# Kernel optimization log

Hardware: AMD Instinct MI355X
Metric: run time of the kernel (lower is better)

Reference implementation:

```python
import jax, jax.numpy as jnp
import numpy as np

S, B, H, T = 1024, 32, 1024, 512


def setup_inputs() -> dict:
    key = jax.random.key(0)
    ks = jax.random.split(key, 7)
    scale = 1.0 / np.sqrt(H)
    return {
        "hidden": jax.random.normal(ks[0], (S, B, H), dtype=jnp.float32),
        "x": jax.random.normal(ks[1], (B, T, H), dtype=jnp.float32),
        "problem_q": jax.random.normal(ks[2], (B, H), dtype=jnp.float32),
        "K_w": jax.random.normal(ks[3], (H, H), dtype=jnp.float32) * scale,
        "K_b": jax.random.normal(ks[4], (H,), dtype=jnp.float32) * scale,
        "V_w": jax.random.normal(ks[5], (H, H), dtype=jnp.float32) * scale,
        "V_b": jax.random.normal(ks[6], (H,), dtype=jnp.float32) * scale,
    }


def reference(hidden, x, problem_q, K_w, K_b, V_w, V_b):
    # hidden: [S, B, H] -> hidden2: [B, S, H]
    hidden2 = jnp.transpose(hidden, (1, 0, 2))
    # Linear projections (torch Linear: y = x @ W.T + b)
    k = jnp.einsum("bsh,kh->bsk", hidden2, K_w) + K_b  # [B, S, H]
    v = jnp.einsum("bsh,kh->bsk", hidden2, V_w) + V_b  # [B, S, H]
    # scores[b,t,s] = x[b,t] . k[b,s]  (QK^T per batch)
    scores = jnp.einsum("bth,bsh->bts", x, k)
    attn = jax.nn.softmax(scores, axis=-1)  # softmax over encoder positions S
    out = jax.nn.sigmoid(jnp.einsum("bts,bsh->bth", attn, v))  # [B, T, H]
    return out
```

## Files before the change

### kernel.cpp

```cpp
#include <hip/hip_runtime.h>

typedef unsigned short u16;
typedef __attribute__((ext_vector_type(8))) short short8;
typedef __attribute__((ext_vector_type(8))) _Float16 half8;
typedef __attribute__((ext_vector_type(4))) float f32x4;
typedef __attribute__((ext_vector_type(4))) u16 u16x4;
typedef __attribute__((ext_vector_type(4))) unsigned int u32x4;

#define DEVINL static __device__ __forceinline__

DEVINL u16 f2bf(float f) {
  unsigned u = __builtin_bit_cast(unsigned, f);
  u += 0x7fffu + ((u >> 16) & 1u);
  return (u16)(u >> 16);
}
DEVINL float bf2f(u16 h) {
  return __builtin_bit_cast(float, ((unsigned)h) << 16);
}
DEVINL u16 f2h(float f) { return __builtin_bit_cast(u16, (_Float16)f); }
DEVINL float h2f(u16 h) { return (float)__builtin_bit_cast(_Float16, h); }

DEVINL void gload16(const void* g, void* l) {
  __builtin_amdgcn_global_load_lds(
      (const __attribute__((address_space(1))) void*)g,
      (__attribute__((address_space(3))) void*)l, 16, 0, 0);
}

#define BAR() asm volatile("s_barrier" ::: "memory")
#define WAIT_VMN(n) asm volatile("s_waitcnt vmcnt(" #n ")" ::: "memory")


__global__ __launch_bounds__(256) void cvt_hidden2_k(const float* __restrict__ hid,
                                                     u16* __restrict__ hf,
                                                     u16* __restrict__ hT) {
  __shared__ u16 tl[64][72];
  const int s0 = blockIdx.x * 64;
  const int h0 = blockIdx.y * 64;
  const int b = blockIdx.z;
  const int t = threadIdx.x;
  const int r = t >> 4;
  const int c4 = (t & 15) * 4;
#pragma unroll
  for (int it = 0; it < 4; ++it) {
    const int s = it * 16 + r;
    const f32x4 v = *(const f32x4*)(hid + ((size_t)(s0 + s) * 32 + b) * 1024 + h0 + c4);
    u16x4 of;
    const int cs = c4 ^ (it << 2);
#pragma unroll
    for (int j = 0; j < 4; ++j) {
      of[j] = f2h(v[j]);
      tl[s][cs + j] = f2bf(v[j]);
    }
    *(u16x4*)(hf + ((size_t)b * 1024 + s0 + s) * 1024 + h0 + c4) = of;
  }
  __syncthreads();
  const int h = t >> 2;
  const int sq = (t & 3) * 16;
  u16 tmp[16] __attribute__((aligned(16)));
#pragma unroll
  for (int i = 0; i < 16; ++i)
    tmp[i] = tl[sq + i][h ^ ((((sq + i) >> 4) & 3) << 2)];
  u16* dst = hT + ((size_t)b * 1024 + h0 + h) * 1024 + s0 + sq;
  *(u32x4*)(dst) = *(const u32x4*)&tmp[0];
  *(u32x4*)(dst + 8) = *(const u32x4*)&tmp[8];
}

__global__ __launch_bounds__(256) void cvt_split_h_k(const float* __restrict__ in,
                                                     u16* __restrict__ hi_o,
                                                     u16* __restrict__ lo_o, long n4) {
  long i = (long)blockIdx.x * 256 + threadIdx.x;
  const long stride = (long)gridDim.x * 256;
  for (; i < n4; i += stride) {
    const f32x4 v = ((const f32x4*)in)[i];
    u16x4 oh, ol;
#pragma unroll
    for (int j = 0; j < 4; ++j) {
      const u16 hi = f2h(v[j]);
      oh[j] = hi;
      ol[j] = f2h(v[j] - h2f(hi));
    }
    ((u16x4*)hi_o)[i] = oh;
    ((u16x4*)lo_o)[i] = ol;
  }
}

__global__ __launch_bounds__(256) void cvt_f32_bf16_k(const float* __restrict__ in,
                                                      u16* __restrict__ out, long n4) {
  long i = (long)blockIdx.x * 256 + threadIdx.x;
  const long stride = (long)gridDim.x * 256;
  for (; i < n4; i += stride) {
    const f32x4 v = ((const f32x4*)in)[i];
    u16x4 o;
#pragma unroll
    for (int j = 0; j < 4; ++j) o[j] = f2bf(v[j]);
    ((u16x4*)out)[i] = o;
  }
}

__global__ __launch_bounds__(256) void cvt_w_t_h_k(const float* __restrict__ in,
                                                   u16* __restrict__ out) {
  __shared__ float tile[64][65];
  const int bh = blockIdx.x * 64;
  const int bj = blockIdx.y * 64;
  const int t = threadIdx.x;
  const int r = t >> 4;
  const int c4 = (t & 15) * 4;
#pragma unroll
  for (int it = 0; it < 4; ++it) {
    const int row = it * 16 + r;
    const f32x4 v = *(const f32x4*)(in + (size_t)(bj + row) * 1024 + bh + c4);
#pragma unroll
    for (int j = 0; j < 4; ++j) tile[c4 + j][row] = v[j];
  }
  __syncthreads();
#pragma unroll
  for (int it = 0; it < 4; ++it) {
    const int hrow = it * 16 + r;
    u16x4 of;
#pragma unroll
    for (int j = 0; j < 4; ++j) of[j] = f2h(tile[hrow][c4 + j]);
    *(u16x4*)(out + (size_t)(bh + hrow) * 1024 + bj + c4) = of;
  }
}

template <int CM>
__global__ __launch_bounds__(512) void gemm2_8ph_k(
    const u16* __restrict__ Ah_, const u16* __restrict__ Al_,
    const u16* __restrict__ B_, void* __restrict__ C0, void* __restrict__ C1) {
  __shared__ u16 lA[3][256 * 64];
  __shared__ u16 lB[3][256 * 32];
  const int bid = blockIdx.x;
  const int swz = (bid & 7) * 32 + (bid >> 3);
  int m0, n0;
  const u16 *Ah, *Al, *Bm;
  float* Cf = nullptr;
  u16 *Chi = nullptr, *Clo = nullptr;
  if (CM == 0) {
    m0 = (swz >> 2) * 256;
    n0 = (swz & 3) * 256;
    Ah = Ah_; Al = Al_; Bm = B_;
    Chi = (u16*)C0; Clo = (u16*)C1;
  } else {
    const int z = swz >> 3;
    m0 = ((swz >> 2) & 1) * 256;
    n0 = (swz & 3) * 256;
    Ah = Ah_ + (size_t)z * 512 * 1024;
    Al = Al_ + (size_t)z * 512 * 1024;
    Bm = B_ + (size_t)z * 1024 * 1024;
    Cf = (float*)C0 + (size_t)z * 512 * 1024;
  }
  const int tid = threadIdx.x;
  const int lane = tid & 63, wid = tid >> 6;
  const int wr = wid >> 2, wc = wid & 3;
  const int fr = lane & 15, fk = lane >> 4;

  f32x4 acc[8][4] = {};

#define STAGEA(pb, kt)                                                         \
  {                                                                            \
    _Pragma("unroll") for (int j = 0; j < 4; ++j) {                            \
      const int slot = j * 512 + tid;                                          \
      const int r = slot >> 3;                                                 \
      const int g = (slot & 7) ^ (r & 7);                                      \
      const u16* src = (g < 4) ? Ah : Al;                                      \
      gload16(src + (size_t)(m0 + r) * 1024 + (kt) * 32 + (g & 3) * 8,         \
              &lA[pb][(j * 512 + wid * 64) * 8]);                              \
    }                                                                          \
  }
#define STAGEB(pb, kt)                                                         \
  {                                                                            \
    _Pragma("unroll") for (int j = 0; j < 2; ++j) {                            \
      const int slot = j * 512 + tid;                                          \
      const int r = slot >> 2;                                                 \
      const int g = (slot & 3) ^ ((r >> 1) & 3);                               \
      gload16(Bm + (size_t)(n0 + r) * 1024 + (kt) * 32 + g * 8,                \
              &lB[pb][(j * 512 + wid * 64) * 8]);                              \
    }                                                                          \
  }

  STAGEA(0, 0);
  STAGEB(0, 0);
  STAGEA(1, 1);
  STAGEB(1, 1);

  int cur = 0;
  for (int t = 0; t < 32; ++t) {
    if (t < 31) {
      WAIT_VMN(6);
    } else {
      WAIT_VMN(0);
    }
    BAR();
    int pre = cur + 2;
    if (pre >= 3) pre -= 3;
    half8 bf[4];
#pragma unroll
    for (int nf = 0; nf < 4; ++nf) {
      const int rn = wc * 64 + nf * 16 + fr;
      const int cn = fk ^ ((rn >> 1) & 3);
      bf[nf] = *(const half8*)&lB[cur][rn * 32 + cn * 8];
    }
    if (t < 30) {
      STAGEA(pre, t + 2);
      STAGEB(pre, t + 2);
    }
#pragma unroll
    for (int ph = 0; ph < 4; ++ph) {
      half8 ah[2], al[2];
#pragma unroll
      for (int i = 0; i < 2; ++i) {
        const int r = wr * 128 + (ph * 2 + i) * 16 + fr;
        const int ch = fk ^ (r & 7);
        ah[i] = *(const half8*)&lA[cur][r * 64 + ch * 8];
        al[i] = *(const half8*)&lA[cur][r * 64 + (ch ^ 4) * 8];
      }
      __builtin_amdgcn_s_setprio(1);
#pragma unroll
      for (int i = 0; i < 2; ++i)
#pragma unroll
        for (int nf = 0; nf < 4; ++nf) {
          acc[ph * 2 + i][nf] =
              __builtin_amdgcn_mfma_f32_16x16x32_f16(ah[i], bf[nf], acc[ph * 2 + i][nf], 0, 0, 0);
          acc[ph * 2 + i][nf] =
              __builtin_amdgcn_mfma_f32_16x16x32_f16(al[i], bf[nf], acc[ph * 2 + i][nf], 0, 0, 0);
        }
      __builtin_amdgcn_s_setprio(0);
    }
    ++cur;
    if (cur == 3) cur = 0;
  }
#undef STAGEA
#undef STAGEB

  const int cb = n0 + wc * 64 + fr;
  const int rb = m0 + wr * 128 + fk * 4;
  if (CM == 0) {
#pragma unroll
    for (int mf = 0; mf < 8; ++mf)
#pragma unroll
      for (int nf = 0; nf < 4; ++nf) {
        const int col = cb + nf * 16;
#pragma unroll
        for (int j = 0; j < 4; ++j) {
          const int row = rb + mf * 16 + j;
          const float kv = acc[mf][nf][j];
          const u16 hi = f2h(kv);
          Chi[(size_t)row * 1024 + col] = hi;
          Clo[(size_t)row * 1024 + col] = f2h(kv - h2f(hi));
        }
      }
  } else {
#pragma unroll
    for (int mf = 0; mf < 8; ++mf)
#pragma unroll
      for (int nf = 0; nf < 4; ++nf) {
        const int col = cb + nf * 16;
#pragma unroll
        for (int j = 0; j < 4; ++j) {
          const int row = rb + mf * 16 + j;
          Cf[(size_t)row * 1024 + col] = acc[mf][nf][j];
        }
      }
  }
}

template <int CM>
__global__ __launch_bounds__(512) void gemm1_8ph_k(
    const u16* __restrict__ A_, const u16* __restrict__ Bt_,
    const float* __restrict__ bias, void* __restrict__ Cout) {
  __shared__ u16 lds[2][2][256 * 64];
  const int bid = blockIdx.x;
  const int swz = (bid & 7) * 32 + (bid >> 3);
  int m0, n0;
  const u16 *A, *Bt;
  float* Cf = nullptr;
  u16* Cb = nullptr;
  if (CM == 0) {
    const int z = swz >> 3;
    m0 = ((swz >> 2) & 1) * 256;
    n0 = (swz & 3) * 256;
    A = A_ + (size_t)z * 512 * 1024;
    Bt = Bt_ + (size_t)z * 1024 * 1024;
    Cb = (u16*)Cout + (size_t)z * 512 * 1024;
  } else {
    m0 = (swz >> 2) * 256;
    n0 = (swz & 3) * 256;
    A = A_; Bt = Bt_;
    Cf = (float*)Cout;
  }
  const int tid = threadIdx.x;
  const int lane = tid & 63, wid = tid >> 6;
  const int wr = wid >> 2, wc = wid & 3;
  const int fr = lane & 15, fk = lane >> 4;

  f32x4 acc[8][4] = {};

#define STAGE1(pb, q, gp, rb, kt)                                              \
  {                                                                            \
    _Pragma("unroll") for (int j = 0; j < 4; ++j) {                            \
      const int slot = j * 512 + tid;                                          \
      const int r = slot >> 3;                                                 \
      const int g = (slot & 7) ^ (r & 7);                                      \
      gload16((gp) + (size_t)((rb) + r) * 1024 + (kt) * 64 + g * 8,            \
              &lds[pb][q][(j * 512 + wid * 64) * 8]);                          \
    }                                                                          \
  }

  STAGE1(0, 0, A, m0, 0);
  STAGE1(0, 1, Bt, n0, 0);

  for (int t = 0; t < 16; ++t) {
    const int p = t & 1;
    WAIT_VMN(0);
    BAR();
    short8 bfr[4][2];
#pragma unroll
    for (int nf = 0; nf < 4; ++nf) {
      const int rn = wc * 64 + nf * 16 + fr;
#pragma unroll
      for (int ks = 0; ks < 2; ++ks) {
        const int g = (ks * 4 + fk) ^ (rn & 7);
        bfr[nf][ks] = *(const short8*)&lds[p][1][rn * 64 + g * 8];
      }
    }
    if (t < 15) {
      STAGE1(p ^ 1, 0, A, m0, t + 1);
      STAGE1(p ^ 1, 1, Bt, n0, t + 1);
    }
#pragma unroll
    for (int ph = 0; ph < 4; ++ph) {
      short8 a[2][2];
#pragma unroll
      for (int i = 0; i < 2; ++i) {
        const int r = wr * 128 + (ph * 2 + i) * 16 + fr;
#pragma unroll
        for (int ks = 0; ks < 2; ++ks) {
          const int g = (ks * 4 + fk) ^ (r & 7);
          a[i][ks] = *(const short8*)&lds[p][0][r * 64 + g * 8];
        }
      }
      __builtin_amdgcn_s_setprio(1);
#pragma unroll
      for (int i = 0; i < 2; ++i)
#pragma unroll
        for (int nf = 0; nf < 4; ++nf) {
          acc[ph * 2 + i][nf] = __builtin_amdgcn_mfma_f32_16x16x32_bf16(
              a[i][0], bfr[nf][0], acc[ph * 2 + i][nf], 0, 0, 0);
          acc[ph * 2 + i][nf] = __builtin_amdgcn_mfma_f32_16x16x32_bf16(
              a[i][1], bfr[nf][1], acc[ph * 2 + i][nf], 0, 0, 0);
        }
      __builtin_amdgcn_s_setprio(0);
    }
  }
#undef STAGE1

  const int cb = n0 + wc * 64 + fr;
  const int rb = m0 + wr * 128 + fk * 4;
  if (CM == 0) {
#pragma unroll
    for (int mf = 0; mf < 8; ++mf)
#pragma unroll
      for (int nf = 0; nf < 4; ++nf) {
        const int col = cb + nf * 16;
#pragma unroll
        for (int j = 0; j < 4; ++j) {
          const int row = rb + mf * 16 + j;
          Cb[(size_t)row * 1024 + col] = f2bf(acc[mf][nf][j]);
        }
      }
  } else {
#pragma unroll
    for (int mf = 0; mf < 8; ++mf)
#pragma unroll
      for (int nf = 0; nf < 4; ++nf) {
        const int col = cb + nf * 16;
        const float bv = bias[col];
#pragma unroll
        for (int j = 0; j < 4; ++j) {
          const int row = rb + mf * 16 + j;
          const float xv = acc[mf][nf][j] + bv;
          Cf[(size_t)row * 1024 + col] = 1.0f / (1.0f + __expf(-xv));
        }
      }
  }
}

__global__ __launch_bounds__(256) void softmax_k(const float* __restrict__ S,
                                                 u16* __restrict__ Attn) {
  const float* rp = S + (size_t)blockIdx.x * 1024;
  const int tid = threadIdx.x;
  const int lane = tid & 63, wid = tid >> 6;
  const f32x4 v = ((const f32x4*)rp)[tid];
  float mx = fmaxf(fmaxf(v[0], v[1]), fmaxf(v[2], v[3]));
#pragma unroll
  for (int off = 32; off; off >>= 1) mx = fmaxf(mx, __shfl_xor(mx, off));
  __shared__ float red[4];
  __shared__ float red2[4];
  if (lane == 0) red[wid] = mx;
  __syncthreads();
  mx = fmaxf(fmaxf(red[0], red[1]), fmaxf(red[2], red[3]));
  const float e0 = __expf(v[0] - mx), e1 = __expf(v[1] - mx);
  const float e2 = __expf(v[2] - mx), e3 = __expf(v[3] - mx);
  float s = (e0 + e1) + (e2 + e3);
#pragma unroll
  for (int off = 32; off; off >>= 1) s += __shfl_xor(s, off);
  if (lane == 0) red2[wid] = s;
  __syncthreads();
  const float inv = 1.0f / (red2[0] + red2[1] + red2[2] + red2[3]);
  u16x4 o;
  o[0] = f2bf(e0 * inv); o[1] = f2bf(e1 * inv); o[2] = f2bf(e2 * inv); o[3] = f2bf(e3 * inv);
  ((u16x4*)(Attn + (size_t)blockIdx.x * 1024))[tid] = o;
}

extern "C" void kernel_launch(void* const* d_in, const int* in_sizes, int n_in,
                              void* d_out, int out_size, void* d_ws, size_t ws_size,
                              hipStream_t stream) {
  const float* hidden = (const float*)d_in[0];
  const float* x = (const float*)d_in[1];
  const float* K_w = (const float*)d_in[3];
  const float* V_w = (const float*)d_in[5];
  const float* V_b = (const float*)d_in[6];

  char* ws = (char*)d_ws;
  u16* hf16 = (u16*)(ws);
  u16* hT = (u16*)(ws + 67108864);
  u16* qhi = (u16*)(ws + 134217728);
  u16* qlo = (u16*)(ws + 167772160);
  float* scoresF = (float*)(ws + 201326592);
  u16* attn = hf16;
  u16* ctx = qhi;
  u16* kwT = (u16*)(ws + 268435456);
  u16* vw = kwT + 1024 * 1024;
  u16* xhi = (u16*)d_out;
  u16* xlo = xhi + 32L * 512 * 1024;
  float* out = (float*)d_out;

  cvt_hidden2_k<<<dim3(16, 16, 32), 256, 0, stream>>>(hidden, hf16, hT);
  cvt_split_h_k<<<2048, 256, 0, stream>>>(x, xhi, xlo, 32L * 512 * 1024 / 4);
  cvt_w_t_h_k<<<dim3(16, 16), 256, 0, stream>>>(K_w, kwT);
  cvt_f32_bf16_k<<<1024, 256, 0, stream>>>(V_w, vw, 1024L * 1024 / 4);
  gemm2_8ph_k<0><<<256, 512, 0, stream>>>(xhi, xlo, kwT, qhi, qlo);
  gemm2_8ph_k<1><<<256, 512, 0, stream>>>(qhi, qlo, hf16, scoresF, nullptr);
  softmax_k<<<16384, 256, 0, stream>>>(scoresF, attn);
  gemm1_8ph_k<0><<<256, 512, 0, stream>>>(attn, hT, nullptr, ctx);
  gemm1_8ph_k<1><<<256, 512, 0, stream>>>(ctx, vw, V_b, out);
}
```

Baseline: 329.9 us.

## Halve gemm2 M-tile to 128 and use double-buffered staging with more blocks

The split-precision gemm2 kernel now computes 128x256 output tiles instead of 256x256, so twice as many blocks (512) are launched. This gives better coverage of the 256 CUs and lower per-block LDS and register use. The LDS pipeline drops from a 3-stage to a 2-stage ring that waits for all loads before each barrier. That removes load/compute overlap depth and lowers data reuse per block in exchange for occupancy.

Measured after the change: 336.2 us. Within noise of the previous version (+1.9%).

```diff
diff --git a/kernel.cpp b/kernel.cpp
--- a/kernel.cpp
+++ b/kernel.cpp
@@ -127,22 +127,22 @@
 __global__ __launch_bounds__(512) void gemm2_8ph_k(
     const u16* __restrict__ Ah_, const u16* __restrict__ Al_,
     const u16* __restrict__ B_, void* __restrict__ C0, void* __restrict__ C1) {
-  __shared__ u16 lA[3][256 * 64];
-  __shared__ u16 lB[3][256 * 32];
+  __shared__ u16 lA[2][128 * 64];
+  __shared__ u16 lB[2][256 * 32];
   const int bid = blockIdx.x;
-  const int swz = (bid & 7) * 32 + (bid >> 3);
+  const int swz = (bid & 7) * 64 + (bid >> 3);
   int m0, n0;
   const u16 *Ah, *Al, *Bm;
   float* Cf = nullptr;
   u16 *Chi = nullptr, *Clo = nullptr;
   if (CM == 0) {
-    m0 = (swz >> 2) * 256;
+    m0 = (swz >> 2) * 128;
     n0 = (swz & 3) * 256;
     Ah = Ah_; Al = Al_; Bm = B_;
     Chi = (u16*)C0; Clo = (u16*)C1;
   } else {
-    const int z = swz >> 3;
-    m0 = ((swz >> 2) & 1) * 256;
+    const int z = swz >> 4;
+    m0 = ((swz >> 2) & 3) * 128;
     n0 = (swz & 3) * 256;
     Ah = Ah_ + (size_t)z * 512 * 1024;
     Al = Al_ + (size_t)z * 512 * 1024;
@@ -154,11 +154,11 @@
   const int wr = wid >> 2, wc = wid & 3;
   const int fr = lane & 15, fk = lane >> 4;
 
-  f32x4 acc[8][4] = {};
+  f32x4 acc[4][4] = {};
 
 #define STAGEA(pb, kt)                                                         \
   {                                                                            \
-    _Pragma("unroll") for (int j = 0; j < 4; ++j) {                            \
+    _Pragma("unroll") for (int j = 0; j < 2; ++j) {                            \
       const int slot = j * 512 + tid;                                          \
       const int r = slot >> 3;                                                 \
       const int g = (slot & 7) ^ (r & 7);                                      \
@@ -180,63 +180,47 @@
 
   STAGEA(0, 0);
   STAGEB(0, 0);
-  STAGEA(1, 1);
-  STAGEB(1, 1);
-
-  int cur = 0;
+
   for (int t = 0; t < 32; ++t) {
-    if (t < 31) {
-      WAIT_VMN(6);
-    } else {
-      WAIT_VMN(0);
-    }
+    const int p = t & 1;
+    WAIT_VMN(0);
     BAR();
-    int pre = cur + 2;
-    if (pre >= 3) pre -= 3;
     half8 bf[4];
 #pragma unroll
     for (int nf = 0; nf < 4; ++nf) {
       const int rn = wc * 64 + nf * 16 + fr;
       const int cn = fk ^ ((rn >> 1) & 3);
-      bf[nf] = *(const half8*)&lB[cur][rn * 32 + cn * 8];
-    }
-    if (t < 30) {
-      STAGEA(pre, t + 2);
-      STAGEB(pre, t + 2);
-    }
-#pragma unroll
-    for (int ph = 0; ph < 4; ++ph) {
-      half8 ah[2], al[2];
-#pragma unroll
-      for (int i = 0; i < 2; ++i) {
-        const int r = wr * 128 + (ph * 2 + i) * 16 + fr;
-        const int ch = fk ^ (r & 7);
-        ah[i] = *(const half8*)&lA[cur][r * 64 + ch * 8];
-        al[i] = *(const half8*)&lA[cur][r * 64 + (ch ^ 4) * 8];
-      }
+      bf[nf] = *(const half8*)&lB[p][rn * 32 + cn * 8];
+    }
+    if (t < 31) {
+      STAGEA(p ^ 1, t + 1);
+      STAGEB(p ^ 1, t + 1);
+    }
+#pragma unroll
+    for (int mf = 0; mf < 4; ++mf) {
+      const int r = wr * 64 + mf * 16 + fr;
+      const int ch = fk ^ (r & 7);
+      const half8 ah = *(const half8*)&lA[p][r * 64 + ch * 8];
+      const half8 al = *(const half8*)&lA[p][r * 64 + (ch ^ 4) * 8];
       __builtin_amdgcn_s_setprio(1);
 #pragma unroll
-      for (int i = 0; i < 2; ++i)
-#pragma unroll
-        for (int nf = 0; nf < 4; ++nf) {
-          acc[ph * 2 + i][nf] =
-              __builtin_amdgcn_mfma_f32_16x16x32_f16(ah[i], bf[nf], acc[ph * 2 + i][nf], 0, 0, 0);
-          acc[ph * 2 + i][nf] =
-              __builtin_amdgcn_mfma_f32_16x16x32_f16(al[i], bf[nf], acc[ph * 2 + i][nf], 0, 0, 0);
-        }
+      for (int nf = 0; nf < 4; ++nf) {
+        acc[mf][nf] =
+            __builtin_amdgcn_mfma_f32_16x16x32_f16(ah, bf[nf], acc[mf][nf], 0, 0, 0);
+        acc[mf][nf] =
+            __builtin_amdgcn_mfma_f32_16x16x32_f16(al, bf[nf], acc[mf][nf], 0, 0, 0);
+      }
       __builtin_amdgcn_s_setprio(0);
     }
-    ++cur;
-    if (cur == 3) cur = 0;
   }
 #undef STAGEA
 #undef STAGEB
 
   const int cb = n0 + wc * 64 + fr;
-  const int rb = m0 + wr * 128 + fk * 4;
+  const int rb = m0 + wr * 64 + fk * 4;
   if (CM == 0) {
 #pragma unroll
-    for (int mf = 0; mf < 8; ++mf)
+    for (int mf = 0; mf < 4; ++mf)
 #pragma unroll
       for (int nf = 0; nf < 4; ++nf) {
         const int col = cb + nf * 16;
@@ -251,7 +235,7 @@
       }
   } else {
 #pragma unroll
-    for (int mf = 0; mf < 8; ++mf)
+    for (int mf = 0; mf < 4; ++mf)
 #pragma unroll
       for (int nf = 0; nf < 4; ++nf) {
         const int col = cb + nf * 16;
@@ -439,8 +423,8 @@
   cvt_split_h_k<<<2048, 256, 0, stream>>>(x, xhi, xlo, 32L * 512 * 1024 / 4);
   cvt_w_t_h_k<<<dim3(16, 16), 256, 0, stream>>>(K_w, kwT);
   cvt_f32_bf16_k<<<1024, 256, 0, stream>>>(V_w, vw, 1024L * 1024 / 4);
-  gemm2_8ph_k<0><<<256, 512, 0, stream>>>(xhi, xlo, kwT, qhi, qlo);
-  gemm2_8ph_k<1><<<256, 512, 0, stream>>>(qhi, qlo, hf16, scoresF, nullptr);
+  gemm2_8ph_k<0><<<512, 512, 0, stream>>>(xhi, xlo, kwT, qhi, qlo);
+  gemm2_8ph_k<1><<<512, 512, 0, stream>>>(qhi, qlo, hf16, scoresF, nullptr);
   softmax_k<<<16384, 256, 0, stream>>>(scoresF, attn);
   gemm1_8ph_k<0><<<256, 512, 0, stream>>>(attn, hT, nullptr, ctx);
   gemm1_8ph_k<1><<<256, 512, 0, stream>>>(ctx, vw, V_b, out);
```
